# Kernel optimization log

Hardware: AMD Instinct MI355X
Metric: run time of the kernel (lower is better)

## Reference

```python
import jax, jax.numpy as jnp
import numpy as np

B, L = 128, 256
VOCAB, E, PF = 50000, 300, 50
C, K, R = 512, 3, 53
D3 = (E + 2 * PF) * 3  # 1200, conv input channels


def setup_inputs() -> dict:
    key = jax.random.key(0)
    ks = jax.random.split(key, 12)
    return {
        "context": jax.random.randint(ks[0], (B, L), 0, VOCAB),
        "subject_idx": jnp.sort(jax.random.randint(ks[1], (B, 2), 0, L), axis=-1),
        "object_idx": jnp.sort(jax.random.randint(ks[2], (B, 2), 0, L), axis=-1),
        "subject_dis": jax.random.randint(ks[3], (B, L), 0, 2 * L),
        "object_dis": jax.random.randint(ks[4], (B, L), 0, 2 * L),
        "embed_table": jax.random.normal(ks[5], (VOCAB, E), dtype=jnp.float32),
        "pos_table": jax.random.normal(ks[6], (2 * L, PF), dtype=jnp.float32),
        "conv_w": jax.random.normal(ks[7], (C, D3, K), dtype=jnp.float32) * (1.0 / np.sqrt(D3 * K)),
        "conv_b": jax.random.normal(ks[8], (C,), dtype=jnp.float32) * 0.01,
        "rela_linear_w": jax.random.normal(ks[9], (R, C), dtype=jnp.float32) * (1.0 / np.sqrt(C)),
        "rela_emb": jax.random.normal(ks[10], (R, C), dtype=jnp.float32),
    }


def _span_mean(wf3, idx):
    # mean of wf3[b, start:end+1, :] per sample, vectorized with a mask
    pos = jnp.arange(wf3.shape[1])[None, :]
    m = ((pos >= idx[:, 0:1]) & (pos <= idx[:, 1:2])).astype(wf3.dtype)  # B,L
    return jnp.einsum("bld,bl->bd", wf3, m) / jnp.sum(m, axis=1, keepdims=True)


def reference(context, subject_idx, object_idx, subject_dis, object_dis,
              embed_table, pos_table, conv_w, conv_b, rela_linear_w, rela_emb):
    emb = embed_table[context]                                            # B,L,E
    posf = jnp.concatenate([pos_table[subject_dis], pos_table[object_dis]], axis=2)
    wf = jnp.concatenate([emb, posf], axis=2)                             # B,L,D
    wp = jnp.pad(wf, ((0, 0), (1, 1), (0, 0)))
    # sliding window concat of [i-1, i, i+1]
    wf3 = jnp.concatenate([wp[:, :-2], wp[:, 1:-1], wp[:, 2:]], axis=2)   # B,L,3D

    subj = _span_mean(wf3, subject_idx)                                   # B,3D
    obj = _span_mean(wf3, object_idx)
    rs = jax.nn.softmax(jnp.einsum("bld,bd->bl", wf3, subj), axis=1)
    ro = jax.nn.softmax(jnp.einsum("bld,bd->bl", wf3, obj), axis=1)
    wf3 = wf3 * ((rs + ro) * 0.5)[:, :, None]

    x = jnp.transpose(wf3, (0, 2, 1))                                     # B,3D,L
    y = jax.lax.conv_general_dilated(x, conv_w, (1,), [(K // 2, K // 2)],
                                     dimension_numbers=("NCH", "OIH", "NCH"))
    sent = jnp.transpose(jnp.tanh(y + conv_b[None, :, None]), (0, 2, 1))  # B,L,C

    attn = jnp.einsum("blr,rc->blc",
                      jnp.einsum("blc,rc->blr", sent, rela_linear_w), rela_emb)
    attn = jax.nn.softmax(attn, axis=1)  # softmax over sequence positions
    wo = jnp.max(sent * attn, axis=1)                                     # B,C
    wo = wo / jnp.maximum(jnp.linalg.norm(wo, axis=1, keepdims=True), 1e-12)
    all_dist = jnp.linalg.norm(wo[:, None, :] - rela_emb[None, :, :], axis=2)  # B,R
    return all_dist
```

## Files before the change

kernel.cpp:

```cpp
#include <hip/hip_runtime.h>
#include <hip/hip_bf16.h>
#include <math.h>

#define B_  128
#define L_  256
#define E_  300
#define PF_ 50
#define D_  400
#define D3_ 1200
#define C_  512
#define KW_ 3
#define R_  53
#define M_  (B_*L_)
#define KP_ 1216
#define K3_ (3*KP_)
#define LROWS_ 258

typedef __attribute__((ext_vector_type(8))) short bf16x8;
typedef __attribute__((ext_vector_type(8))) unsigned short u16x8;
typedef __attribute__((ext_vector_type(4))) float f32x4;

__device__ __forceinline__ unsigned short f2bf(float f) {
    union { float f; unsigned u; } x; x.f = f;
    unsigned r = x.u + 0x7FFF + ((x.u >> 16) & 1);
    return (unsigned short)(r >> 16);
}
__device__ __forceinline__ float bf2f(unsigned short u) {
    union { unsigned u; float f; } x; x.u = ((unsigned)u) << 16;
    return x.f;
}

__device__ __forceinline__ void gld16(const void* g, void* l) {
    __builtin_amdgcn_global_load_lds(
        (const __attribute__((address_space(1))) void*)g,
        (__attribute__((address_space(3))) void*)l, 16, 0, 0);
}

__device__ __forceinline__ void stage_half(const unsigned short* g, size_t gstr,
                                           unsigned short* ldsb, int t) {
#pragma unroll
    for (int s = 0; s < 2; ++s) {
        int row = s * 128 + (t >> 2);
        int lslot = (t & 3) ^ ((t >> 2) & 3);
        gld16(g + (size_t)row * gstr + lslot * 8, (char*)ldsb + s * 8192 + t * 16);
    }
}

__global__ void prep_wpT_kernel(const float* __restrict__ conv_w, unsigned short* __restrict__ WpT) {
    int idx = blockIdx.x * blockDim.x + threadIdx.x;
    if (idx >= C_ * K3_) return;
    int c = idx / K3_, q = idx % K3_;
    int k = q / KP_, ch = q % KP_;
    WpT[idx] = (ch < D3_) ? f2bf(conv_w[c * (D3_ * KW_) + ch * KW_ + k]) : (unsigned short)0;
}

__global__ void prep_mT_kernel(const float* __restrict__ rlw, const float* __restrict__ re,
                               unsigned short* __restrict__ MmatT) {
    int idx = blockIdx.x * blockDim.x + threadIdx.x;
    if (idx >= C_ * C_) return;
    int n = idx / C_, k = idx % C_;
    float acc = 0.f;
    for (int r = 0; r < R_; ++r)
        acc += rlw[r * C_ + k] * re[r * C_ + n];
    MmatT[idx] = f2bf(acc);
}

__global__ void build_wf_kernel(const int* __restrict__ ctx, const int* __restrict__ sdis,
                                const int* __restrict__ odis, const float* __restrict__ emb,
                                const float* __restrict__ pos, float* __restrict__ wf) {
    const int total = M_ * D_;
    for (int idx = blockIdx.x * blockDim.x + threadIdx.x; idx < total;
         idx += gridDim.x * blockDim.x) {
        int d = idx % D_;
        int bt = idx / D_;
        float v;
        if (d < E_)            v = emb[(long)ctx[bt] * E_ + d];
        else if (d < E_ + PF_) v = pos[sdis[bt] * PF_ + (d - E_)];
        else                   v = pos[odis[bt] * PF_ + (d - E_ - PF_)];
        wf[idx] = v;
    }
}

__global__ void prefix_wf_kernel(const float* __restrict__ wf, float* __restrict__ Pref) {
    int idx = blockIdx.x * blockDim.x + threadIdx.x;
    if (idx >= B_ * D_) return;
    int b = idx / D_, d = idx % D_;
    const float* src = wf + (size_t)(b << 8) * D_ + d;
    float* dst = Pref + (size_t)(b << 8) * D_ + d;
    float acc = 0.f;
    for (int t = 0; t < L_; ++t) {
        acc += src[(size_t)t * D_];
        dst[(size_t)t * D_] = acc;
    }
}

__global__ void span_mean_kernel(const float* __restrict__ Pref,
                                 const int* __restrict__ sidx, const int* __restrict__ oidx,
                                 float* __restrict__ SS, float* __restrict__ OS) {
    int idx = blockIdx.x * blockDim.x + threadIdx.x;
    if (idx >= B_ * 3 * D_) return;
    int b = idx / (3 * D_);
    int r = idx % (3 * D_);
    int j = r / D_, d = r % D_;

    {
        int s0 = sidx[b * 2], s1 = sidx[b * 2 + 1];
        float inv = 1.f / (float)(s1 - s0 + 1);
        int lo = s0 + j - 1, hi = s1 + j - 1;
        int loc = lo < 0 ? 0 : lo;
        int hic = hi > (L_ - 1) ? (L_ - 1) : hi;
        float sum = 0.f;
        if (loc <= hic) {
            float a = Pref[((size_t)((b << 8) + hic)) * D_ + d];
            float c = (loc > 0) ? Pref[((size_t)((b << 8) + loc - 1)) * D_ + d] : 0.f;
            sum = a - c;
        }
        SS[((size_t)(b * 3 + j)) * D_ + d] = sum * inv;
    }
    {
        int s0 = oidx[b * 2], s1 = oidx[b * 2 + 1];
        float inv = 1.f / (float)(s1 - s0 + 1);
        int lo = s0 + j - 1, hi = s1 + j - 1;
        int loc = lo < 0 ? 0 : lo;
        int hic = hi > (L_ - 1) ? (L_ - 1) : hi;
        float sum = 0.f;
        if (loc <= hic) {
            float a = Pref[((size_t)((b << 8) + hic)) * D_ + d];
            float c = (loc > 0) ? Pref[((size_t)((b << 8) + loc - 1)) * D_ + d] : 0.f;
            sum = a - c;
        }
        OS[((size_t)(b * 3 + j)) * D_ + d] = sum * inv;
    }
}

__global__ __launch_bounds__(256) void dots_kernel(
    const float* __restrict__ wf, const float* __restrict__ SS, const float* __restrict__ OS,
    float* __restrict__ dsb, float* __restrict__ ddb) {
    const int wave = threadIdx.x >> 6, lane = threadIdx.x & 63;
    const int g = blockIdx.x * 4 + wave;
    const int b = g >> 8, t = g & 255;
    float ds = 0.f, dd = 0.f;
#pragma unroll
    for (int j = 0; j < 3; ++j) {
        int u = t + j - 1;
        if ((unsigned)u < (unsigned)L_) {
            const float4* w  = (const float4*)(wf + ((size_t)((b << 8) + u)) * D_);
            const float4* ss = (const float4*)(SS + ((size_t)(b * 3 + j)) * D_);
            const float4* oo = (const float4*)(OS + ((size_t)(b * 3 + j)) * D_);
            for (int q = lane; q < D_ / 4; q += 64) {
                float4 wv = w[q], sv = ss[q], ov = oo[q];
                ds += wv.x * sv.x + wv.y * sv.y + wv.z * sv.z + wv.w * sv.w;
                dd += wv.x * ov.x + wv.y * ov.y + wv.z * ov.z + wv.w * ov.w;
            }
        }
    }
#pragma unroll
    for (int off = 32; off > 0; off >>= 1) {
        ds += __shfl_down(ds, off);
        dd += __shfl_down(dd, off);
    }
    if (lane == 0) { dsb[g] = ds; ddb[g] = dd; }
}

__global__ __launch_bounds__(256) void softmax_s_kernel(
    const float* __restrict__ dsb, const float* __restrict__ ddb, float* __restrict__ s) {
    const int b = blockIdx.x, tid = threadIdx.x;
    __shared__ float red[256];
    float ds = dsb[(b << 8) + tid];
    float dd = ddb[(b << 8) + tid];

    red[tid] = ds; __syncthreads();
    for (int st = 128; st > 0; st >>= 1) {
        if (tid < st) red[tid] = fmaxf(red[tid], red[tid + st]);
        __syncthreads();
    }
    float ms = red[0]; __syncthreads();
    float es = expf(ds - ms);
    red[tid] = es; __syncthreads();
    for (int st = 128; st > 0; st >>= 1) {
        if (tid < st) red[tid] += red[tid + st];
        __syncthreads();
    }
    float zs = red[0]; __syncthreads();

    red[tid] = dd; __syncthreads();
    for (int st = 128; st > 0; st >>= 1) {
        if (tid < st) red[tid] = fmaxf(red[tid], red[tid + st]);
        __syncthreads();
    }
    float mo = red[0]; __syncthreads();
    float eo = expf(dd - mo);
    red[tid] = eo; __syncthreads();
    for (int st = 128; st > 0; st >>= 1) {
        if (tid < st) red[tid] += red[tid + st];
        __syncthreads();
    }
    float zo = red[0];

    s[(b << 8) + tid] = 0.5f * (es / zs + eo / zo);
}

__global__ void build_xsp_kernel(const float* __restrict__ wf, const float* __restrict__ s,
                                 unsigned short* __restrict__ XSp) {
    const int CH8 = KP_ / 8;
    int idx = blockIdx.x * blockDim.x + threadIdx.x;
    const int total = B_ * LROWS_ * CH8;
    if (idx >= total) return;
    int chunk = idx % CH8;
    int rb = idx / CH8;
    int row = rb % LROWS_;
    int b = rb / LROWS_;

    u16x8 out = {0,0,0,0,0,0,0,0};
    int t = row - 1;
    int ch0 = chunk * 8;
    if ((unsigned)t < (unsigned)L_ && ch0 < D3_) {
        int j = ch0 / D_;
        int d0 = ch0 - j * D_;
        int u = t + j - 1;
        if ((unsigned)u < (unsigned)L_) {
            float sc = s[(b << 8) + t];
            const float* w = wf + ((size_t)((b << 8) + u)) * D_ + d0;
#pragma unroll
            for (int q = 0; q < 8; ++q) out[q] = f2bf(sc * w[q]);
        }
    }
    *(u16x8*)&XSp[((size_t)(b * LROWS_ + row)) * KP_ + ch0] = out;
}

template<int MODE>
__global__ __launch_bounds__(512, 2) void gemm8_kernel(
    const unsigned short* __restrict__ Aglob, const unsigned short* __restrict__ Bglob,
    const float* __restrict__ conv_b, unsigned short* __restrict__ outb,
    float* __restrict__ outf) {
    extern __shared__ unsigned short lds[];
    const int tid = threadIdx.x;
    const int lane = tid & 63;
    const int wave = tid >> 6;
    const int wr = wave >> 2;
    const int wc = wave & 3;
    const int bx = blockIdx.x;
    const int blockM = bx * 256;
    const int blockN = blockIdx.y * 256;
    const int l15 = lane & 15;
    const int kswz = (((lane >> 4) ^ (lane & 3)) << 3);
    const int NT = (MODE == 0) ? (K3_ / 64) : (C_ / 64);

    const size_t Astr = (MODE == 0) ? (size_t)KP_ : (size_t)C_;
    const size_t Bstr = (MODE == 0) ? (size_t)K3_ : (size_t)C_;

    auto abase = [&](int kt) -> const unsigned short* {
        if constexpr (MODE == 0) {
            int tap = kt / KP_, ch0 = kt - tap * KP_;
            return Aglob + (size_t)(bx * LROWS_ + tap) * KP_ + ch0;
        } else {
            return Aglob + (size_t)blockM * C_ + kt;
        }
    };
    auto bbase = [&](int kt) -> const unsigned short* {
        return Bglob + (size_t)blockN * Bstr + kt;
    };

    f32x4 acc[8][4] = {};

    {
        const unsigned short* Ag = abase(0);
        const unsigned short* Bg = bbase(0);
        stage_half(Ag,      Astr, &lds[0],            tid);
        stage_half(Bg,      Bstr, &lds[32768],        tid);
        stage_half(Ag + 32, Astr, &lds[8192],         tid);
        stage_half(Bg + 32, Bstr, &lds[32768 + 8192], tid);
    }
    asm volatile("s_waitcnt vmcnt(4)" ::: "memory");
    __builtin_amdgcn_s_barrier();

    int cur = 0;
    for (int kt = 0; kt < NT * 64; kt += 64, cur ^= 1) {
        const int nxt = cur ^ 1;
        int ktn = kt + 64;
        if (ktn >= NT * 64) ktn = 0;
        const unsigned short* Agn = abase(ktn);
        const unsigned short* Bgn = bbase(ktn);
        unsigned short* Alds = &lds[nxt * 16384];
        unsigned short* Blds = &lds[32768 + nxt * 16384];
        const unsigned short* Ac = &lds[cur * 16384 + (size_t)(wr * 128 + l15) * 32 + kswz];
        const unsigned short* Bc = &lds[32768 + cur * 16384 + (size_t)(wc * 64 + l15) * 32 + kswz];

        bf16x8 a[8], b0, b1;

#pragma unroll
        for (int mi = 0; mi < 8; ++mi) a[mi] = *(const bf16x8*)&Ac[mi * 512];
        b0 = *(const bf16x8*)&Bc[0];
        b1 = *(const bf16x8*)&Bc[512];
        stage_half(Agn, Astr, Alds, tid);
        __builtin_amdgcn_s_barrier();
        asm volatile("s_waitcnt lgkmcnt(0)" ::: "memory");
        __builtin_amdgcn_s_setprio(1);
#pragma unroll
        for (int mi = 0; mi < 8; ++mi) {
            acc[mi][0] = __builtin_amdgcn_mfma_f32_16x16x32_bf16(a[mi], b0, acc[mi][0], 0, 0, 0);
            acc[mi][1] = __builtin_amdgcn_mfma_f32_16x16x32_bf16(a[mi], b1, acc[mi][1], 0, 0, 0);
        }
        __builtin_amdgcn_s_setprio(0);
        __builtin_amdgcn_s_barrier();

        b0 = *(const bf16x8*)&Bc[1024];
        b1 = *(const bf16x8*)&Bc[1536];
        stage_half(Bgn, Bstr, Blds, tid);
        __builtin_amdgcn_s_barrier();
        asm volatile("s_waitcnt lgkmcnt(0)" ::: "memory");
        __builtin_amdgcn_s_setprio(1);
#pragma unroll
        for (int mi = 0; mi < 8; ++mi) {
            acc[mi][2] = __builtin_amdgcn_mfma_f32_16x16x32_bf16(a[mi], b0, acc[mi][2], 0, 0, 0);
            acc[mi][3] = __builtin_amdgcn_mfma_f32_16x16x32_bf16(a[mi], b1, acc[mi][3], 0, 0, 0);
        }
        __builtin_amdgcn_s_setprio(0);
        asm volatile("s_waitcnt vmcnt(4)" ::: "memory");
        __builtin_amdgcn_s_barrier();

#pragma unroll
        for (int mi = 0; mi < 8; ++mi) a[mi] = *(const bf16x8*)&Ac[8192 + mi * 512];
        b0 = *(const bf16x8*)&Bc[8192];
        b1 = *(const bf16x8*)&Bc[8192 + 512];
        stage_half(Agn + 32, Astr, Alds + 8192, tid);
        __builtin_amdgcn_s_barrier();
        asm volatile("s_waitcnt lgkmcnt(0)" ::: "memory");
        __builtin_amdgcn_s_setprio(1);
#pragma unroll
        for (int mi = 0; mi < 8; ++mi) {
            acc[mi][0] = __builtin_amdgcn_mfma_f32_16x16x32_bf16(a[mi], b0, acc[mi][0], 0, 0, 0);
            acc[mi][1] = __builtin_amdgcn_mfma_f32_16x16x32_bf16(a[mi], b1, acc[mi][1], 0, 0, 0);
        }
        __builtin_amdgcn_s_setprio(0);
        __builtin_amdgcn_s_barrier();

        b0 = *(const bf16x8*)&Bc[8192 + 1024];
        b1 = *(const bf16x8*)&Bc[8192 + 1536];
        stage_half(Bgn + 32, Bstr, Blds + 8192, tid);
        __builtin_amdgcn_s_barrier();
        asm volatile("s_waitcnt lgkmcnt(0)" ::: "memory");
        __builtin_amdgcn_s_setprio(1);
#pragma unroll
        for (int mi = 0; mi < 8; ++mi) {
            acc[mi][2] = __builtin_amdgcn_mfma_f32_16x16x32_bf16(a[mi], b0, acc[mi][2], 0, 0, 0);
            acc[mi][3] = __builtin_amdgcn_mfma_f32_16x16x32_bf16(a[mi], b1, acc[mi][3], 0, 0, 0);
        }
        __builtin_amdgcn_s_setprio(0);
        asm volatile("s_waitcnt vmcnt(4)" ::: "memory");
        __builtin_amdgcn_s_barrier();
    }

    asm volatile("s_waitcnt vmcnt(0)" ::: "memory");

    const int r4 = ((lane >> 4) << 2);
#pragma unroll
    for (int mi = 0; mi < 8; ++mi) {
#pragma unroll
        for (int nj = 0; nj < 4; ++nj) {
            const int col = blockN + wc * 64 + nj * 16 + l15;
            const int row0 = blockM + wr * 128 + mi * 16 + r4;
            if constexpr (MODE == 0) {
                float bias = conv_b[col];
#pragma unroll
                for (int r = 0; r < 4; ++r)
                    outb[(size_t)(row0 + r) * C_ + col] = f2bf(tanhf(acc[mi][nj][r] + bias));
            } else {
#pragma unroll
                for (int r = 0; r < 4; ++r)
                    outf[(size_t)(row0 + r) * C_ + col] = acc[mi][nj][r];
            }
        }
    }
}

__global__ __launch_bounds__(256) void softmax_wo_kernel(
    const float* __restrict__ P, const unsigned short* __restrict__ sent,
    float* __restrict__ wo) {
    const int b = blockIdx.x;
    const int c = blockIdx.y * 256 + threadIdx.x;
    const float* Pb = P + ((size_t)(b << 8)) * C_ + c;
    const unsigned short* Sb = sent + ((size_t)(b << 8)) * C_ + c;
    float m = -INFINITY;
    for (int l = 0; l < L_; ++l) m = fmaxf(m, Pb[(size_t)l * C_]);
    float z = 0.f, wmax = -INFINITY;
    for (int l = 0; l < L_; ++l) {
        float e = expf(Pb[(size_t)l * C_] - m);
        z += e;
        wmax = fmaxf(wmax, bf2f(Sb[(size_t)l * C_]) * e);
    }
    wo[b * C_ + c] = wmax / z;
}

__global__ __launch_bounds__(256) void final_kernel(
    const float* __restrict__ wo, const float* __restrict__ re, float* __restrict__ out) {
    const int b = blockIdx.x, tid = threadIdx.x;
    __shared__ float won[C_];
    __shared__ float red[256];
    float p = 0.f;
    for (int c = tid; c < C_; c += 256) {
        float v = wo[b * C_ + c];
        p += v * v;
    }
    red[tid] = p; __syncthreads();
    for (int st = 128; st > 0; st >>= 1) {
        if (tid < st) red[tid] += red[tid + st];
        __syncthreads();
    }
    float inv = 1.f / fmaxf(sqrtf(red[0]), 1e-12f);
    for (int c = tid; c < C_; c += 256) won[c] = wo[b * C_ + c] * inv;
    __syncthreads();
    const int wv = tid >> 6, lane = tid & 63;
    for (int r = wv; r < R_; r += 4) {
        float acc2 = 0.f;
        for (int c = lane; c < C_; c += 64) {
            float dlt = won[c] - re[r * C_ + c];
            acc2 += dlt * dlt;
        }
        for (int off = 32; off > 0; off >>= 1) acc2 += __shfl_down(acc2, off);
        if (lane == 0) out[b * R_ + r] = sqrtf(acc2);
    }
}

extern "C" void kernel_launch(void* const* d_in, const int* in_sizes, int n_in,
                              void* d_out, int out_size, void* d_ws, size_t ws_size,
                              hipStream_t stream) {
    const int* context     = (const int*)d_in[0];
    const int* subject_idx = (const int*)d_in[1];
    const int* object_idx  = (const int*)d_in[2];
    const int* subject_dis = (const int*)d_in[3];
    const int* object_dis  = (const int*)d_in[4];
    const float* embed_table = (const float*)d_in[5];
    const float* pos_table   = (const float*)d_in[6];
    const float* conv_w      = (const float*)d_in[7];
    const float* conv_b      = (const float*)d_in[8];
    const float* rlw         = (const float*)d_in[9];
    const float* re          = (const float*)d_in[10];
    float* out = (float*)d_out;

    char* ws = (char*)d_ws;
    size_t off = 0;
    auto alloc = [&](size_t bytes) {
        void* p = ws + off;
        off = (off + bytes + 255) & ~(size_t)255;
        return p;
    };
    float* wf            = (float*)alloc((size_t)M_ * D_ * 4);
    float* s             = (float*)alloc((size_t)M_ * 4);
    unsigned short* XSp  = (unsigned short*)alloc((size_t)B_ * LROWS_ * KP_ * 2);
    unsigned short* WpT  = (unsigned short*)alloc((size_t)C_ * K3_ * 2);
    unsigned short* MmatT= (unsigned short*)alloc((size_t)C_ * C_ * 2);
    unsigned short* sent = (unsigned short*)alloc((size_t)M_ * C_ * 2);
    float* wo            = (float*)alloc((size_t)B_ * C_ * 4);
    float* SS            = (float*)alloc((size_t)B_ * 3 * D_ * 4);
    float* OS            = (float*)alloc((size_t)B_ * 3 * D_ * 4);
    float* dsb           = (float*)alloc((size_t)M_ * 4);
    float* ddb           = (float*)alloc((size_t)M_ * 4);
    float* Pref = (float*)XSp;
    float* P    = (float*)XSp;

    (void)hipFuncSetAttribute((const void*)gemm8_kernel<0>,
                              hipFuncAttributeMaxDynamicSharedMemorySize, 131072);
    (void)hipFuncSetAttribute((const void*)gemm8_kernel<1>,
                              hipFuncAttributeMaxDynamicSharedMemorySize, 131072);

    prep_wpT_kernel<<<(C_ * K3_ + 255) / 256, 256, 0, stream>>>(conv_w, WpT);
    prep_mT_kernel<<<(C_ * C_ + 255) / 256, 256, 0, stream>>>(rlw, re, MmatT);
    build_wf_kernel<<<4096, 256, 0, stream>>>(context, subject_dis, object_dis,
                                              embed_table, pos_table, wf);
    prefix_wf_kernel<<<(B_ * D_ + 255) / 256, 256, 0, stream>>>(wf, Pref);
    span_mean_kernel<<<(B_ * 3 * D_ + 255) / 256, 256, 0, stream>>>(Pref, subject_idx,
                                                                    object_idx, SS, OS);
    dots_kernel<<<M_ / 4, 256, 0, stream>>>(wf, SS, OS, dsb, ddb);
    softmax_s_kernel<<<B_, 256, 0, stream>>>(dsb, ddb, s);
    build_xsp_kernel<<<(B_ * LROWS_ * (KP_ / 8) + 255) / 256, 256, 0, stream>>>(wf, s, XSp);
    gemm8_kernel<0><<<dim3(M_ / 256, C_ / 256), 512, 131072, stream>>>(
        XSp, WpT, conv_b, sent, nullptr);
    gemm8_kernel<1><<<dim3(M_ / 256, C_ / 256), 512, 131072, stream>>>(
        sent, MmatT, nullptr, nullptr, P);
    softmax_wo_kernel<<<dim3(B_, 2), 256, 0, stream>>>(P, sent, wo);
    final_kernel<<<B_, 256, 0, stream>>>(wo, re, out);
}
```

Before: 331.9 us.

## Stage full 64-wide K tiles with XOR swizzle and one barrier per iteration

Reworks the MFMA GEMM's LDS staging. Each wave now loads a slice of a full 64-wide K tile for A and B into a swizzled 8-slot layout, replacing half-tile loads spread across four phases. The per-iteration barriers and explicit vmcnt waits collapse into a single __syncthreads at the end of the iteration, meant to cut synchronization stalls between MFMA phases. The trade-off is that outstanding prefetches are fully drained each iteration rather than kept partially in flight, which may reduce load/compute overlap.

```diff
diff --git a/kernel.cpp b/kernel.cpp
--- a/kernel.cpp
+++ b/kernel.cpp
@@ -36,16 +36,6 @@
         (__attribute__((address_space(3))) void*)l, 16, 0, 0);
 }
 
-__device__ __forceinline__ void stage_half(const unsigned short* g, size_t gstr,
-                                           unsigned short* ldsb, int t) {
-#pragma unroll
-    for (int s = 0; s < 2; ++s) {
-        int row = s * 128 + (t >> 2);
-        int lslot = (t & 3) ^ ((t >> 2) & 3);
-        gld16(g + (size_t)row * gstr + lslot * 8, (char*)ldsb + s * 8192 + t * 16);
-    }
-}
-
 __global__ void prep_wpT_kernel(const float* __restrict__ conv_w, unsigned short* __restrict__ WpT) {
     int idx = blockIdx.x * blockDim.x + threadIdx.x;
     if (idx >= C_ * K3_) return;
@@ -240,61 +230,69 @@
     const int wr = wave >> 2;
     const int wc = wave & 3;
     const int bx = blockIdx.x;
-    const int blockM = bx * 256;
     const int blockN = blockIdx.y * 256;
     const int l15 = lane & 15;
-    const int kswz = (((lane >> 4) ^ (lane & 3)) << 3);
     const int NT = (MODE == 0) ? (K3_ / 64) : (C_ / 64);
-
     const size_t Astr = (MODE == 0) ? (size_t)KP_ : (size_t)C_;
     const size_t Bstr = (MODE == 0) ? (size_t)K3_ : (size_t)C_;
 
-    auto abase = [&](int kt) -> const unsigned short* {
+    const int arole = wc;
+    const int bhalf = wc >> 1;
+    const int brole = wr * 2 + (wc & 1);
+
+    const int acol0 = (((lane >> 4) + 0) ^ (l15 & 7)) * 8;
+    const int acol1 = (((lane >> 4) + 4) ^ (l15 & 7)) * 8;
+    const int bro = (wc & 1) * 64;
+
+    auto stageA = [&](int kt, int buf) {
+        const unsigned short* gb;
         if constexpr (MODE == 0) {
             int tap = kt / KP_, ch0 = kt - tap * KP_;
-            return Aglob + (size_t)(bx * LROWS_ + tap) * KP_ + ch0;
+            gb = Aglob + ((size_t)(bx * LROWS_ + wr * 128 + tap)) * KP_ + ch0;
         } else {
-            return Aglob + (size_t)blockM * C_ + kt;
+            gb = Aglob + ((size_t)(bx * 256 + wr * 128)) * C_ + kt;
+        }
+        unsigned short* pb = &lds[(buf * 2 + wr) * 8192];
+#pragma unroll
+        for (int i = 0; i < 4; ++i) {
+            int sl = arole * 256 + i * 64 + lane;
+            int row = sl >> 3, p = sl & 7;
+            int colg = p ^ (row & 7);
+            gld16(gb + (size_t)row * Astr + colg * 8, (char*)pb + sl * 16);
         }
     };
-    auto bbase = [&](int kt) -> const unsigned short* {
-        return Bglob + (size_t)blockN * Bstr + kt;
+    auto stageB = [&](int kt, int buf) {
+        const unsigned short* gb = Bglob + ((size_t)(blockN + bhalf * 128)) * Bstr + kt;
+        unsigned short* pb = &lds[32768 + (buf * 2 + bhalf) * 8192];
+#pragma unroll
+        for (int i = 0; i < 4; ++i) {
+            int sl = brole * 256 + i * 64 + lane;
+            int row = sl >> 3, p = sl & 7;
+            int colg = p ^ (row & 7);
+            gld16(gb + (size_t)row * Bstr + colg * 8, (char*)pb + sl * 16);
+        }
     };
 
     f32x4 acc[8][4] = {};
 
-    {
-        const unsigned short* Ag = abase(0);
-        const unsigned short* Bg = bbase(0);
-        stage_half(Ag,      Astr, &lds[0],            tid);
-        stage_half(Bg,      Bstr, &lds[32768],        tid);
-        stage_half(Ag + 32, Astr, &lds[8192],         tid);
-        stage_half(Bg + 32, Bstr, &lds[32768 + 8192], tid);
-    }
-    asm volatile("s_waitcnt vmcnt(4)" ::: "memory");
-    __builtin_amdgcn_s_barrier();
+    stageA(0, 0);
+    stageB(0, 0);
+    __syncthreads();
 
     int cur = 0;
     for (int kt = 0; kt < NT * 64; kt += 64, cur ^= 1) {
-        const int nxt = cur ^ 1;
         int ktn = kt + 64;
         if (ktn >= NT * 64) ktn = 0;
-        const unsigned short* Agn = abase(ktn);
-        const unsigned short* Bgn = bbase(ktn);
-        unsigned short* Alds = &lds[nxt * 16384];
-        unsigned short* Blds = &lds[32768 + nxt * 16384];
-        const unsigned short* Ac = &lds[cur * 16384 + (size_t)(wr * 128 + l15) * 32 + kswz];
-        const unsigned short* Bc = &lds[32768 + cur * 16384 + (size_t)(wc * 64 + l15) * 32 + kswz];
+        const unsigned short* Ap = &lds[(cur * 2 + wr) * 8192];
+        const unsigned short* Bp = &lds[32768 + (cur * 2 + bhalf) * 8192];
 
         bf16x8 a[8], b0, b1;
 
 #pragma unroll
-        for (int mi = 0; mi < 8; ++mi) a[mi] = *(const bf16x8*)&Ac[mi * 512];
-        b0 = *(const bf16x8*)&Bc[0];
-        b1 = *(const bf16x8*)&Bc[512];
-        stage_half(Agn, Astr, Alds, tid);
-        __builtin_amdgcn_s_barrier();
-        asm volatile("s_waitcnt lgkmcnt(0)" ::: "memory");
+        for (int mi = 0; mi < 8; ++mi) a[mi] = *(const bf16x8*)&Ap[(mi * 16 + l15) * 64 + acol0];
+        b0 = *(const bf16x8*)&Bp[(bro + 0 * 16 + l15) * 64 + acol0];
+        b1 = *(const bf16x8*)&Bp[(bro + 1 * 16 + l15) * 64 + acol0];
+        stageA(ktn, cur ^ 1);
         __builtin_amdgcn_s_setprio(1);
 #pragma unroll
         for (int mi = 0; mi < 8; ++mi) {
@@ -302,13 +300,10 @@
             acc[mi][1] = __builtin_amdgcn_mfma_f32_16x16x32_bf16(a[mi], b1, acc[mi][1], 0, 0, 0);
         }
         __builtin_amdgcn_s_setprio(0);
-        __builtin_amdgcn_s_barrier();
-
-        b0 = *(const bf16x8*)&Bc[1024];
-        b1 = *(const bf16x8*)&Bc[1536];
-        stage_half(Bgn, Bstr, Blds, tid);
-        __builtin_amdgcn_s_barrier();
-        asm volatile("s_waitcnt lgkmcnt(0)" ::: "memory");
+
+        b0 = *(const bf16x8*)&Bp[(bro + 2 * 16 + l15) * 64 + acol0];
+        b1 = *(const bf16x8*)&Bp[(bro + 3 * 16 + l15) * 64 + acol0];
+        stageB(ktn, cur ^ 1);
         __builtin_amdgcn_s_setprio(1);
 #pragma unroll
         for (int mi = 0; mi < 8; ++mi) {
@@ -316,16 +311,11 @@
             acc[mi][3] = __builtin_amdgcn_mfma_f32_16x16x32_bf16(a[mi], b1, acc[mi][3], 0, 0, 0);
         }
         __builtin_amdgcn_s_setprio(0);
-        asm volatile("s_waitcnt vmcnt(4)" ::: "memory");
-        __builtin_amdgcn_s_barrier();
-
-#pragma unroll
-        for (int mi = 0; mi < 8; ++mi) a[mi] = *(const bf16x8*)&Ac[8192 + mi * 512];
-        b0 = *(const bf16x8*)&Bc[8192];
-        b1 = *(const bf16x8*)&Bc[8192 + 512];
-        stage_half(Agn + 32, Astr, Alds + 8192, tid);
-        __builtin_amdgcn_s_barrier();
-        asm volatile("s_waitcnt lgkmcnt(0)" ::: "memory");
+
+#pragma unroll
+        for (int mi = 0; mi < 8; ++mi) a[mi] = *(const bf16x8*)&Ap[(mi * 16 + l15) * 64 + acol1];
+        b0 = *(const bf16x8*)&Bp[(bro + 0 * 16 + l15) * 64 + acol1];
+        b1 = *(const bf16x8*)&Bp[(bro + 1 * 16 + l15) * 64 + acol1];
         __builtin_amdgcn_s_setprio(1);
 #pragma unroll
         for (int mi = 0; mi < 8; ++mi) {
@@ -333,13 +323,9 @@
             acc[mi][1] = __builtin_amdgcn_mfma_f32_16x16x32_bf16(a[mi], b1, acc[mi][1], 0, 0, 0);
         }
         __builtin_amdgcn_s_setprio(0);
-        __builtin_amdgcn_s_barrier();
-
-        b0 = *(const bf16x8*)&Bc[8192 + 1024];
-        b1 = *(const bf16x8*)&Bc[8192 + 1536];
-        stage_half(Bgn + 32, Bstr, Blds + 8192, tid);
-        __builtin_amdgcn_s_barrier();
-        asm volatile("s_waitcnt lgkmcnt(0)" ::: "memory");
+
+        b0 = *(const bf16x8*)&Bp[(bro + 2 * 16 + l15) * 64 + acol1];
+        b1 = *(const bf16x8*)&Bp[(bro + 3 * 16 + l15) * 64 + acol1];
         __builtin_amdgcn_s_setprio(1);
 #pragma unroll
         for (int mi = 0; mi < 8; ++mi) {
@@ -347,11 +333,9 @@
             acc[mi][3] = __builtin_amdgcn_mfma_f32_16x16x32_bf16(a[mi], b1, acc[mi][3], 0, 0, 0);
         }
         __builtin_amdgcn_s_setprio(0);
-        asm volatile("s_waitcnt vmcnt(4)" ::: "memory");
-        __builtin_amdgcn_s_barrier();
-    }
-
-    asm volatile("s_waitcnt vmcnt(0)" ::: "memory");
+
+        __syncthreads();
+    }
 
     const int r4 = ((lane >> 4) << 2);
 #pragma unroll
@@ -359,7 +343,7 @@
 #pragma unroll
         for (int nj = 0; nj < 4; ++nj) {
             const int col = blockN + wc * 64 + nj * 16 + l15;
-            const int row0 = blockM + wr * 128 + mi * 16 + r4;
+            const int row0 = bx * 256 + wr * 128 + mi * 16 + r4;
             if constexpr (MODE == 0) {
                 float bias = conv_b[col];
 #pragma unroll
```

Result: faster. 315.0 us (-5.1%).
